# Kernel optimization log

Hardware: AMD Instinct MI355X
Metric: run time of the kernel (lower is better)

The kernel has to match this reference:

```python
import jax, jax.numpy as jnp
import numpy as np

N_NODES = 3      # fixed by the reshape to (3*batch_size, out_feats)
N_EDGES = 8
BN_EPS = 1e-5


def setup_inputs() -> dict:
    key = jax.random.key(0)
    k_h, k_w, k_b, k_src, k_dst = jax.random.split(key, 5)
    B, F_in, F_out = 262144, 128, 128
    h = jax.random.normal(k_h, (B, N_NODES, F_in), dtype=jnp.float32)
    # reset_parameters uses uniform_ init on the Linear weight
    W = jax.random.uniform(k_w, (F_out, F_in), dtype=jnp.float32)
    b = jax.random.normal(k_b, (F_out,), dtype=jnp.float32) * 0.01
    gamma = jnp.ones((N_NODES,), dtype=jnp.float32)   # BatchNorm1d(nCell) weight
    beta = jnp.zeros((N_NODES,), dtype=jnp.float32)   # BatchNorm1d(nCell) bias
    src = jax.random.randint(k_src, (N_EDGES,), 0, N_NODES)
    dst = jax.random.randint(k_dst, (N_EDGES,), 0, N_NODES)
    return {"h": h, "W": W, "b": b, "gamma": gamma, "beta": beta,
            "src": src, "dst": dst}


def reference(h, W, b, gamma, beta, src, dst):
    # Linear over feature dim: (B, N, F_in) -> (B, N, F_out)
    x = jnp.einsum('bnf,of->bno', h, W) + b
    # BatchNorm1d(nCell): channel dim is node dim (axis 1); training-mode
    # batch statistics over (batch, feature) dims.
    mean = jnp.mean(x, axis=(0, 2), keepdims=True)
    var = jnp.var(x, axis=(0, 2), keepdims=True)
    x = (x - mean) * jax.lax.rsqrt(var + BN_EPS)
    x = x * gamma[None, :, None] + beta[None, :, None]
    # copy_src + sum == h'[v] = sum over edges (u->v) of h[u];
    # since the same tiny graph is batched B times, this is a 3x3
    # adjacency-count matmul applied per batch element.
    A = jnp.zeros((N_NODES, N_NODES), dtype=x.dtype).at[dst, src].add(1.0)
    out = jnp.einsum('vu,buf->bvf', A, x)
    return jax.nn.relu(out)
```

## Files before the change

### kernel.cpp

```cpp
#include <hip/hip_runtime.h>
#include <hip/hip_bf16.h>

typedef __attribute__((ext_vector_type(8))) short short8;
typedef __attribute__((ext_vector_type(4))) float f32x4;

#define WSTRIDE 136

__device__ __forceinline__ unsigned short f2bf(float x){
    union { float f; unsigned u; } v; v.f = x;
    unsigned r = v.u + 0x7FFFu + ((v.u >> 16) & 1u);
    return (unsigned short)(r >> 16);
}

__device__ __forceinline__ void stageW(const float* __restrict__ W, unsigned short* Wlds, int tid){
    for (int idx = tid; idx < 2048; idx += 256){
        int row = idx >> 4, ch = idx & 15;
        const f32x4* sp = (const f32x4*)(W + row*128 + ch*8);
        f32x4 p0 = sp[0], p1 = sp[1];
        short8 s;
        s[0]=(short)f2bf(p0[0]); s[1]=(short)f2bf(p0[1]);
        s[2]=(short)f2bf(p0[2]); s[3]=(short)f2bf(p0[3]);
        s[4]=(short)f2bf(p1[0]); s[5]=(short)f2bf(p1[1]);
        s[6]=(short)f2bf(p1[2]); s[7]=(short)f2bf(p1[3]);
        *(short8*)(&Wlds[row*WSTRIDE + ch*8]) = s;
    }
}

__global__ __launch_bounds__(256) void k1_gemm_stats(
    const float* __restrict__ h, const float* __restrict__ W,
    const float* __restrict__ bias, double* __restrict__ partials,
    int nChunks, int nBlocks)
{
    __shared__ __align__(16) unsigned short Wlds[128*WSTRIDE];
    __shared__ __align__(16) float biasLds[128];
    __shared__ float wred[4][6];
    int tid = threadIdx.x;
    stageW(W, Wlds, tid);
    if (tid < 128) biasLds[tid] = bias[tid];
    __syncthreads();

    int lane = tid & 63, w = tid >> 6;
    int m = lane & 15, kg = lane >> 4;
    int pr = w >> 1;
    int hh = w & 1;
    int ob0 = hh*64;
    float s0=0.f,s1=0.f,s2=0.f,q0=0.f,q1=0.f,q2=0.f;
    f32x4 zero = {0.f,0.f,0.f,0.f};

    f32x4 fbuf[8];
    short8 abuf[4];

    auto issueL = [&](int chunk){
        const float* hrow = h + ((long)(chunk*32 + pr*16 + m))*128;
        #pragma unroll
        for (int kc=0;kc<4;kc++){
            fbuf[kc*2]   = *(const f32x4*)(hrow + kc*32 + kg*8);
            fbuf[kc*2+1] = *(const f32x4*)(hrow + kc*32 + kg*8 + 4);
        }
    };
    auto convert = [&](){
        #pragma unroll
        for (int kc=0;kc<4;kc++){
            f32x4 p0 = fbuf[kc*2], p1 = fbuf[kc*2+1];
            short8 a;
            a[0]=(short)f2bf(p0[0]); a[1]=(short)f2bf(p0[1]);
            a[2]=(short)f2bf(p0[2]); a[3]=(short)f2bf(p0[3]);
            a[4]=(short)f2bf(p1[0]); a[5]=(short)f2bf(p1[1]);
            a[6]=(short)f2bf(p1[2]); a[7]=(short)f2bf(p1[3]);
            abuf[kc] = a;
        }
    };
    auto compute = [&](int chunk){
        int row = chunk*32 + pr*16 + m;
        f32x4 acc[4];
        #pragma unroll
        for (int nt=0;nt<4;nt++) acc[nt]=zero;
        #pragma unroll
        for (int kc=0;kc<4;kc++){
            int k0 = kc*32 + kg*8;
            #pragma unroll
            for (int nt=0;nt<4;nt++){
                short8 wf = *(const short8*)(&Wlds[(ob0+nt*16+m)*WSTRIDE + k0]);
                acc[nt] = __builtin_amdgcn_mfma_f32_16x16x32_bf16(wf, abuf[kc], acc[nt], 0, 0, 0);
            }
        }
        float cs = 0.f, cq = 0.f;
        #pragma unroll
        for (int nt=0;nt<4;nt++){
            f32x4 bo = *(const f32x4*)(&biasLds[ob0 + nt*16 + kg*4]);
            float v0 = acc[nt][0] + bo[0];
            float v1 = acc[nt][1] + bo[1];
            float v2 = acc[nt][2] + bo[2];
            float v3 = acc[nt][3] + bo[3];
            cs += (v0+v1)+(v2+v3);
            cq += (v0*v0+v1*v1)+(v2*v2+v3*v3);
        }
        int node = row % 3;
        s0 += (node==0)?cs:0.f; q0 += (node==0)?cq:0.f;
        s1 += (node==1)?cs:0.f; q1 += (node==1)?cq:0.f;
        s2 += (node==2)?cs:0.f; q2 += (node==2)?cq:0.f;
    };

    int c = blockIdx.x;
    bool have = (c < nChunks);
    if (have){ issueL(c); convert(); }
    while (have){
        int cn = c + nBlocks;
        bool haveN = (cn < nChunks);
        if (haveN) issueL(cn);
        compute(c);
        if (haveN) convert();
        c = cn; have = haveN;
    }

    #pragma unroll
    for (int off=32; off>0; off>>=1){
        s0 += __shfl_down(s0,off,64); s1 += __shfl_down(s1,off,64); s2 += __shfl_down(s2,off,64);
        q0 += __shfl_down(q0,off,64); q1 += __shfl_down(q1,off,64); q2 += __shfl_down(q2,off,64);
    }
    if (lane==0){
        wred[w][0]=s0; wred[w][1]=s1; wred[w][2]=s2;
        wred[w][3]=q0; wred[w][4]=q1; wred[w][5]=q2;
    }
    __syncthreads();
    if (tid < 6){
        double t = (double)wred[0][tid]+(double)wred[1][tid]+(double)wred[2][tid]+(double)wred[3][tid];
        partials[(long)blockIdx.x*6 + tid] = t;
    }
}

__global__ void k_finalize(const double* __restrict__ partials, int nb,
    const float* __restrict__ gamma, const float* __restrict__ beta,
    const int* __restrict__ src, const int* __restrict__ dst, int nE,
    double cnt, float* __restrict__ coef)
{
    __shared__ double red[256];
    __shared__ double tot[6];
    int tid = threadIdx.x;
    double loc[6] = {0,0,0,0,0,0};
    for (int i = tid; i < nb; i += 256){
        #pragma unroll
        for (int c=0;c<6;c++) loc[c] += partials[(long)i*6+c];
    }
    for (int c=0;c<6;c++){
        red[tid] = loc[c];
        __syncthreads();
        for (int s=128;s>0;s>>=1){
            if (tid < s) red[tid] += red[tid+s];
            __syncthreads();
        }
        if (tid==0) tot[c] = red[0];
        __syncthreads();
    }
    if (tid==0){
        float A[9];
        #pragma unroll
        for (int i=0;i<9;i++) A[i]=0.f;
        for (int e=0;e<nE;e++) A[dst[e]*3 + src[e]] += 1.f;
        float meanv[3], rsv[3];
        #pragma unroll
        for (int n=0;n<3;n++){
            double mean = tot[n]/cnt;
            double var  = tot[3+n]/cnt - mean*mean;
            double rs   = 1.0/sqrt(var + 1e-5);
            meanv[n]=(float)mean; rsv[n]=(float)rs;
        }
        #pragma unroll
        for (int v=0;v<3;v++){
            float c_=0.f, rS=0.f;
            #pragma unroll
            for (int u=0;u<3;u++){
                float s_ = A[v*3+u]*gamma[u]*rsv[u];
                coef[v*3+u] = s_;
                rS += s_;
                c_ += A[v*3+u]*(beta[u] - gamma[u]*rsv[u]*meanv[u]);
            }
            coef[9+v]  = c_;
            coef[12+v] = rS;
        }
    }
}

__global__ __launch_bounds__(256) void k3_recompute(
    const float* __restrict__ h, const float* __restrict__ W,
    const float* __restrict__ bias, const float* __restrict__ coef,
    float* __restrict__ out, int Bq, int ntiles, int nBlocks)
{
    __shared__ __align__(16) unsigned short Wlds[128*WSTRIDE];
    __shared__ __align__(16) float biasLds[128];
    __shared__ float coefLds[15];
    int tid = threadIdx.x;
    stageW(W, Wlds, tid);
    if (tid < 128) biasLds[tid] = bias[tid];
    if (tid < 15)  coefLds[tid] = coef[tid];
    __syncthreads();

    int lane = tid & 63, w = tid >> 6;
    int m = lane & 15, kg = lane >> 4;

    float s00=coefLds[0], s01=coefLds[1], s02=coefLds[2];
    float s10=coefLds[3], s11=coefLds[4], s12=coefLds[5];
    float s20=coefLds[6], s21=coefLds[7], s22=coefLds[8];
    float c0=coefLds[9],  c1=coefLds[10], c2=coefLds[11];
    float r0s=coefLds[12], r1s=coefLds[13], r2s=coefLds[14];
    f32x4 zero = {0.f,0.f,0.f,0.f};

    for (int t = ntiles - 1 - blockIdx.x; t >= 0; t -= nBlocks){
        int bq0 = t*64 + w*16;
        int bqv = bq0 + m;
        bool ok = bqv < Bq;
        int bqL = ok ? bqv : (Bq-1);
        const float* hb = h + (long)bqL*384;

        f32x4 acc[3][8];
        #pragma unroll
        for (int v=0;v<3;v++)
            #pragma unroll
            for (int nt=0;nt<8;nt++) acc[v][nt]=zero;

        #pragma unroll
        for (int kc=0;kc<4;kc++){
            int k0 = kc*32 + kg*8;
            f32x4 x0  = *(const f32x4*)(hb + k0);
            f32x4 x0b = *(const f32x4*)(hb + k0 + 4);
            f32x4 x1  = *(const f32x4*)(hb + 128 + k0);
            f32x4 x1b = *(const f32x4*)(hb + 128 + k0 + 4);
            f32x4 x2  = *(const f32x4*)(hb + 256 + k0);
            f32x4 x2b = *(const f32x4*)(hb + 256 + k0 + 4);
            short8 a0, a1, a2;
            #pragma unroll
            for (int i=0;i<4;i++){
                a0[i]   = (short)f2bf(s00*x0[i]  + s01*x1[i]  + s02*x2[i]);
                a0[4+i] = (short)f2bf(s00*x0b[i] + s01*x1b[i] + s02*x2b[i]);
                a1[i]   = (short)f2bf(s10*x0[i]  + s11*x1[i]  + s12*x2[i]);
                a1[4+i] = (short)f2bf(s10*x0b[i] + s11*x1b[i] + s12*x2b[i]);
                a2[i]   = (short)f2bf(s20*x0[i]  + s21*x1[i]  + s22*x2[i]);
                a2[4+i] = (short)f2bf(s20*x0b[i] + s21*x1b[i] + s22*x2b[i]);
            }
            #pragma unroll
            for (int nt=0;nt<8;nt++){
                short8 wf = *(const short8*)(&Wlds[(nt*16+m)*WSTRIDE + k0]);
                acc[0][nt] = __builtin_amdgcn_mfma_f32_16x16x32_bf16(wf, a0, acc[0][nt], 0,0,0);
                acc[1][nt] = __builtin_amdgcn_mfma_f32_16x16x32_bf16(wf, a1, acc[1][nt], 0,0,0);
                acc[2][nt] = __builtin_amdgcn_mfma_f32_16x16x32_bf16(wf, a2, acc[2][nt], 0,0,0);
            }
        }
        float* ob = out + (long)bqv*384 + kg*4;
        #pragma unroll
        for (int v=0;v<3;v++){
            float cv = (v==0)?c0:((v==1)?c1:c2);
            float rv = (v==0)?r0s:((v==1)?r1s:r2s);
            #pragma unroll
            for (int nt=0;nt<8;nt++){
                f32x4 bo = *(const f32x4*)(&biasLds[nt*16 + kg*4]);
                f32x4 o4;
                #pragma unroll
                for (int j=0;j<4;j++)
                    o4[j] = fmaxf(acc[v][nt][j] + bo[j]*rv + cv, 0.f);
                if (ok) __builtin_nontemporal_store(o4, (f32x4*)(ob + v*128 + nt*16));
            }
        }
    }
}

extern "C" void kernel_launch(void* const* d_in, const int* in_sizes, int n_in,
                              void* d_out, int out_size, void* d_ws, size_t ws_size,
                              hipStream_t stream) {
    const float* h     = (const float*)d_in[0];
    const float* W     = (const float*)d_in[1];
    const float* bias  = (const float*)d_in[2];
    const float* gamma = (const float*)d_in[3];
    const float* beta  = (const float*)d_in[4];
    const int*   src   = (const int*)d_in[5];
    const int*   dst   = (const int*)d_in[6];
    float* out = (float*)d_out;

    long rows = (long)in_sizes[0] / 128;
    int  Bq   = (int)(rows / 3);
    int nE = in_sizes[5];
    double cnt = (double)Bq * 128.0;

    int nChunks = (int)(rows / 32);
    int NB1 = 1024;
    if ((size_t)NB1*48 + 64 > ws_size){
        NB1 = (int)((ws_size > 112 ? (ws_size - 64) : (size_t)48) / 48);
        if (NB1 < 1) NB1 = 1;
        if (NB1 > 1024) NB1 = 1024;
    }
    double* partials = (double*)d_ws;
    float* coef = (float*)((char*)d_ws + (size_t)NB1*48);

    k1_gemm_stats<<<NB1, 256, 0, stream>>>(h, W, bias, partials, nChunks, NB1);
    k_finalize<<<1, 256, 0, stream>>>(partials, NB1, gamma, beta, src, dst, nE, cnt, coef);
    int ntiles = (Bq + 63) / 64;
    int NB3 = ntiles < 1024 ? ntiles : 1024;
    k3_recompute<<<NB3, 256, 0, stream>>>(h, W, bias, coef, out, Bq, ntiles, NB3);
}
```

Measured before the change: 277.1 us.

## Stream h through an async LDS ring and keep W fragments in registers

The stats GEMM kernel no longer stages bf16 W in LDS. Each wave converts its W fragments and bias once into registers. Input rows of h are fetched with global_load_lds into a swizzled four-slot LDS ring, kept two tiles ahead, using explicit vmcnt waits and a barrier per tile, then converted to bf16 from LDS before the MFMAs. The aim is deeper memory-level parallelism on the bandwidth-bound pass over h and fewer LDS reads for W, at the cost of more VGPRs, 64 KB of LDS per block and a grid cut from 1024 to 512 blocks.

```diff
diff --git a/kernel.cpp b/kernel.cpp
--- a/kernel.cpp
+++ b/kernel.cpp
@@ -29,69 +29,81 @@
 __global__ __launch_bounds__(256) void k1_gemm_stats(
     const float* __restrict__ h, const float* __restrict__ W,
     const float* __restrict__ bias, double* __restrict__ partials,
-    int nChunks, int nBlocks)
+    int ntiles, int nBlocks)
 {
-    __shared__ __align__(16) unsigned short Wlds[128*WSTRIDE];
-    __shared__ __align__(16) float biasLds[128];
+    __shared__ __align__(16) char ring[65536];
     __shared__ float wred[4][6];
     int tid = threadIdx.x;
-    stageW(W, Wlds, tid);
-    if (tid < 128) biasLds[tid] = bias[tid];
-    __syncthreads();
-
     int lane = tid & 63, w = tid >> 6;
     int m = lane & 15, kg = lane >> 4;
     int pr = w >> 1;
     int hh = w & 1;
-    int ob0 = hh*64;
+    int ob0 = hh * 64;
+
+    short8 wfr[4][4];
+    f32x4 bo[4];
+    #pragma unroll
+    for (int nt=0;nt<4;nt++){
+        bo[nt] = *(const f32x4*)(bias + ob0 + nt*16 + kg*4);
+        #pragma unroll
+        for (int kc=0;kc<4;kc++){
+            const f32x4* wp = (const f32x4*)(W + (long)(ob0 + nt*16 + m)*128 + kc*32 + kg*8);
+            f32x4 p0 = wp[0], p1 = wp[1];
+            short8 s;
+            s[0]=(short)f2bf(p0[0]); s[1]=(short)f2bf(p0[1]);
+            s[2]=(short)f2bf(p0[2]); s[3]=(short)f2bf(p0[3]);
+            s[4]=(short)f2bf(p1[0]); s[5]=(short)f2bf(p1[1]);
+            s[6]=(short)f2bf(p1[2]); s[7]=(short)f2bf(p1[3]);
+            wfr[nt][kc] = s;
+        }
+    }
+
     float s0=0.f,s1=0.f,s2=0.f,q0=0.f,q1=0.f,q2=0.f;
     f32x4 zero = {0.f,0.f,0.f,0.f};
 
-    f32x4 fbuf[8];
-    short8 abuf[4];
-
-    auto issueL = [&](int chunk){
-        const float* hrow = h + ((long)(chunk*32 + pr*16 + m))*128;
+    auto issueSlot = [&](int t, int slot){
+        const char* gbase = (const char*)h + ((size_t)t*32 + (size_t)pr*16)*512;
+        char* lbase = ring + (pr*4 + slot)*8192;
+        #pragma unroll
+        for (int jj=0;jj<4;jj++){
+            int j = hh*4 + jj;
+            int d = j*64 + lane;
+            int row = d >> 5, g = d & 31;
+            const char* src = gbase + row*512 + ((g ^ (row & 7)) << 4);
+            __builtin_amdgcn_global_load_lds(
+                (const __attribute__((address_space(1))) void*)src,
+                (__attribute__((address_space(3))) void*)(lbase + j*1024),
+                16, 0, 0);
+        }
+    };
+
+    auto computeSlot = [&](int t, int slot){
+        int row = t*32 + pr*16 + m;
+        const char* lb = ring + (pr*4 + slot)*8192 + m*512;
+        f32x4 acc[4];
+        #pragma unroll
+        for (int nt=0;nt<4;nt++) acc[nt]=zero;
         #pragma unroll
         for (int kc=0;kc<4;kc++){
-            fbuf[kc*2]   = *(const f32x4*)(hrow + kc*32 + kg*8);
-            fbuf[kc*2+1] = *(const f32x4*)(hrow + kc*32 + kg*8 + 4);
-        }
-    };
-    auto convert = [&](){
-        #pragma unroll
-        for (int kc=0;kc<4;kc++){
-            f32x4 p0 = fbuf[kc*2], p1 = fbuf[kc*2+1];
+            int sg = kc*8 + kg*2;
+            f32x4 p0 = *(const f32x4*)(lb + (( sg      ^ (m&7))<<4));
+            f32x4 p1 = *(const f32x4*)(lb + (((sg + 1) ^ (m&7))<<4));
             short8 a;
             a[0]=(short)f2bf(p0[0]); a[1]=(short)f2bf(p0[1]);
             a[2]=(short)f2bf(p0[2]); a[3]=(short)f2bf(p0[3]);
             a[4]=(short)f2bf(p1[0]); a[5]=(short)f2bf(p1[1]);
             a[6]=(short)f2bf(p1[2]); a[7]=(short)f2bf(p1[3]);
-            abuf[kc] = a;
-        }
-    };
-    auto compute = [&](int chunk){
-        int row = chunk*32 + pr*16 + m;
-        f32x4 acc[4];
-        #pragma unroll
-        for (int nt=0;nt<4;nt++) acc[nt]=zero;
-        #pragma unroll
-        for (int kc=0;kc<4;kc++){
-            int k0 = kc*32 + kg*8;
-            #pragma unroll
-            for (int nt=0;nt<4;nt++){
-                short8 wf = *(const short8*)(&Wlds[(ob0+nt*16+m)*WSTRIDE + k0]);
-                acc[nt] = __builtin_amdgcn_mfma_f32_16x16x32_bf16(wf, abuf[kc], acc[nt], 0, 0, 0);
-            }
+            #pragma unroll
+            for (int nt=0;nt<4;nt++)
+                acc[nt] = __builtin_amdgcn_mfma_f32_16x16x32_bf16(wfr[nt][kc], a, acc[nt], 0, 0, 0);
         }
         float cs = 0.f, cq = 0.f;
         #pragma unroll
         for (int nt=0;nt<4;nt++){
-            f32x4 bo = *(const f32x4*)(&biasLds[ob0 + nt*16 + kg*4]);
-            float v0 = acc[nt][0] + bo[0];
-            float v1 = acc[nt][1] + bo[1];
-            float v2 = acc[nt][2] + bo[2];
-            float v3 = acc[nt][3] + bo[3];
+            float v0 = acc[nt][0] + bo[nt][0];
+            float v1 = acc[nt][1] + bo[nt][1];
+            float v2 = acc[nt][2] + bo[nt][2];
+            float v3 = acc[nt][3] + bo[nt][3];
             cs += (v0+v1)+(v2+v3);
             cq += (v0*v0+v1*v1)+(v2*v2+v3*v3);
         }
@@ -101,16 +113,23 @@
         s2 += (node==2)?cs:0.f; q2 += (node==2)?cq:0.f;
     };
 
-    int c = blockIdx.x;
-    bool have = (c < nChunks);
-    if (have){ issueL(c); convert(); }
-    while (have){
-        int cn = c + nBlocks;
-        bool haveN = (cn < nChunks);
-        if (haveN) issueL(cn);
-        compute(c);
-        if (haveN) convert();
-        c = cn; have = haveN;
+    int bid = blockIdx.x;
+    int n = (bid < ntiles) ? ((ntiles - 1 - bid)/nBlocks + 1) : 0;
+
+    if (n > 0) issueSlot(bid, 0);
+    if (n > 1) issueSlot(bid + nBlocks, 1);
+    for (int i=0;i<n;i++){
+        if (i+2 < n){
+            issueSlot(bid + (i+2)*nBlocks, (i+2)&3);
+            asm volatile("s_waitcnt vmcnt(8)" ::: "memory");
+        } else if (i+1 < n){
+            asm volatile("s_waitcnt vmcnt(4)" ::: "memory");
+        } else {
+            asm volatile("s_waitcnt vmcnt(0)" ::: "memory");
+        }
+        __builtin_amdgcn_sched_barrier(0);
+        __builtin_amdgcn_s_barrier();
+        computeSlot(bid + i*nBlocks, i&3);
     }
 
     #pragma unroll
@@ -280,17 +299,17 @@
     int nE = in_sizes[5];
     double cnt = (double)Bq * 128.0;
 
-    int nChunks = (int)(rows / 32);
-    int NB1 = 1024;
+    int ntiles32 = (int)(rows / 32);
+    int NB1 = 512;
     if ((size_t)NB1*48 + 64 > ws_size){
         NB1 = (int)((ws_size > 112 ? (ws_size - 64) : (size_t)48) / 48);
         if (NB1 < 1) NB1 = 1;
-        if (NB1 > 1024) NB1 = 1024;
+        if (NB1 > 512) NB1 = 512;
     }
     double* partials = (double*)d_ws;
     float* coef = (float*)((char*)d_ws + (size_t)NB1*48);
 
-    k1_gemm_stats<<<NB1, 256, 0, stream>>>(h, W, bias, partials, nChunks, NB1);
+    k1_gemm_stats<<<NB1, 256, 0, stream>>>(h, W, bias, partials, ntiles32, NB1);
     k_finalize<<<1, 256, 0, stream>>>(partials, NB1, gamma, beta, src, dst, nE, cnt, coef);
     int ntiles = (Bq + 63) / 64;
     int NB3 = ntiles < 1024 ? ntiles : 1024;
```

Result: faster. 252.7 us (-8.8%).
